# Performance work log

Measured on AMD Instinct MI355X. Metric: run time of the kernel, lower is better.

## Reference

```python
import jax, jax.numpy as jnp
import numpy as np

B, C, HID, H, W = 32, 256, 128, 32, 32  # batch, input_dim, hidden_dim, grid


def conv1x1(x, Wt, b):
    # 1x1 Conv2d == channel-mixing matmul. x: [B,Cin,H,W], Wt: [Cout,Cin]
    return jnp.einsum('oc,bchw->bohw', Wt, x) + b[None, :, None, None]


def setup_inputs() -> dict:
    key = jax.random.key(0)
    ks = jax.random.split(key, 18)
    p = lambda k, shape: (jax.random.normal(k, shape, jnp.float32) * 0.02)
    return {
        'h': jax.random.normal(ks[0], (B, C, H, W), jnp.float32),
        'm': jax.random.normal(ks[1], (B, C, H, W), jnp.float32),
        'Wq': p(ks[2], (HID, C)),  'bq': p(ks[3], (HID,)),
        'Wk': p(ks[4], (HID, C)),  'bk': p(ks[5], (HID,)),
        'Wv': p(ks[6], (C, C)),    'bv': p(ks[7], (C,)),
        'Wk2': p(ks[8], (HID, C)), 'bk2': p(ks[9], (HID,)),
        'Wv2': p(ks[10], (C, C)),  'bv2': p(ks[11], (C,)),
        'Wz': p(ks[12], (2 * C, 2 * C)), 'bz': p(ks[13], (2 * C,)),
        'Wm': p(ks[14], (3 * C, 3 * C)), 'bm': p(ks[15], (3 * C,)),
    }


def reference(h, m, Wq, bq, Wk, bk, Wv, bv, Wk2, bk2, Wv2, bv2, Wz, bz, Wm, bm):
    Bb, Cc, Hh, Ww = h.shape
    HW = Hh * Ww
    # shared query from h: [B, HID, HW]
    q = conv1x1(h, Wq, bq).reshape(Bb, -1, HW)
    # self-attention branch over h (unscaled logits, as in original)
    kh = conv1x1(h, Wk, bk).reshape(Bb, -1, HW)
    A_h = jax.nn.softmax(jnp.einsum('bdp,bdq->bpq', q, kh), axis=-1)  # [B,HW,HW]
    vh = conv1x1(h, Wv, bv).reshape(Bb, Cc, HW)
    Z_h = jnp.einsum('bpq,bcq->bcp', A_h, vh).reshape(Bb, Cc, Hh, Ww)
    # cross-attention branch over memory m with shared q
    km = conv1x1(m, Wk2, bk2).reshape(Bb, -1, HW)
    A_m = jax.nn.softmax(jnp.einsum('bdp,bdq->bpq', q, km), axis=-1)
    vm = conv1x1(m, Wv2, bv2).reshape(Bb, Cc, HW)
    Z_m = jnp.einsum('bpq,bcq->bcp', A_m, vm).reshape(Bb, Cc, Hh, Ww)
    # fuse, then LSTM-style gating
    Z = conv1x1(jnp.concatenate([Z_h, Z_m], axis=1), Wz, bz)          # [B,2C,H,W]
    comb = conv1x1(jnp.concatenate([Z, h], axis=1), Wm, bm)           # [B,3C,H,W]
    mo, mg, mi = jnp.split(comb, 3, axis=1)
    mi = jax.nn.sigmoid(mi)
    new_m = (1.0 - mi) * m + mi * jnp.tanh(mg)
    new_h = jax.nn.sigmoid(mo) * new_m
    return new_h, new_m
```

## Files before the change

kernel.cpp:

```cpp
#include <hip/hip_runtime.h>
#include <hip/hip_bf16.h>

typedef __bf16  v8bf __attribute__((ext_vector_type(8)));
typedef float   v4f  __attribute__((ext_vector_type(4)));
typedef float   f4   __attribute__((ext_vector_type(4)));
typedef unsigned short us8 __attribute__((ext_vector_type(8)));
typedef unsigned short us4 __attribute__((ext_vector_type(4)));
typedef unsigned int u32;

#define BATCH 32
#define CDIM  256
#define HW    1024

#define OFF_HBT 0L
#define OFF_MBT (OFF_HBT + 16777216L)
#define OFF_QKH (OFF_MBT + 16777216L)
#define OFF_QKM (OFF_QKH + 16777216L)
#define OFF_VH  (OFF_QKM + 8388608L)
#define OFF_VM  (OFF_VH  + 16777216L)
#define OFF_ZCT (OFF_VM  + 16777216L)
#define OFF_W   (OFF_ZCT + 33554432L)
#define OFF_B   (OFF_W   + 3866624L)
#define WS_TOTAL (OFF_B + 2944L * 4)
#define W_QK  0
#define W_K2  65536
#define W_V   98304
#define W_V2  163840
#define W_M   491520
#define W_ZT  1081344
#define W_F   1343488
#define B_QK  0
#define B_K2  256
#define B_V   384
#define B_V2  640
#define B_F   2176

__device__ inline unsigned short f2u(float x) {
    __hip_bfloat16 h = __float2bfloat16(x);
    union { __hip_bfloat16 h; unsigned short u; } cv; cv.h = h; return cv.u;
}
__device__ inline float u2f(unsigned short u) {
    union { unsigned short u; __hip_bfloat16 h; } cv; cv.u = u; return __bfloat162float(cv.h);
}
__device__ inline float sigmoidf_(float x) {
    x = fminf(fmaxf(x, -30.f), 30.f);
    return 1.f / (1.f + __expf(-x));
}
__device__ inline float tanhf_(float x) {
    x = fminf(fmaxf(x, -15.f), 15.f);
    float e = __expf(2.f * x);
    return (e - 1.f) / (e + 1.f);
}
__device__ inline void glds16(const unsigned short* g, unsigned short* l) {
    __builtin_amdgcn_global_load_lds(
        (const __attribute__((address_space(1))) u32*)g,
        (__attribute__((address_space(3))) u32*)l, 16, 0, 0);
}

__global__ __launch_bounds__(256)
void prep(const float* __restrict__ hsrc, const float* __restrict__ msrc,
          const float* __restrict__ Wq, const float* __restrict__ Wk,
          const float* __restrict__ Wv, const float* __restrict__ Wk2,
          const float* __restrict__ Wv2, const float* __restrict__ Wz,
          const float* __restrict__ Wm,
          const float* __restrict__ bq, const float* __restrict__ bk,
          const float* __restrict__ bk2, const float* __restrict__ bv,
          const float* __restrict__ bv2, const float* __restrict__ bz,
          const float* __restrict__ bm,
          char* __restrict__ ws)
{
    __shared__ float t[64][68];
    unsigned short* wdst = (unsigned short*)(ws + OFF_W);
    float*          bdst = (float*)(ws + OFF_B);
    const int bid = blockIdx.x;
    const int tid = threadIdx.x;

    if (bid < 6025) {
        const int gid = bid * 256 + tid;
        if (gid < 1081344) {
            const float* s; int off;
            if      (gid <   32768) { s = Wq;  off = gid; }
            else if (gid <   65536) { s = Wk;  off = gid -   32768; }
            else if (gid <   98304) { s = Wk2; off = gid -   65536; }
            else if (gid <  163840) { s = Wv;  off = gid -   98304; }
            else if (gid <  229376) { s = Wv2; off = gid -  163840; }
            else if (gid <  491520) { s = Wz;  off = gid -  229376; }
            else                    { s = Wm;  off = gid -  491520; }
            wdst[gid] = f2u(s[off]);
        } else if (gid < 1343488) {
            const int idx = gid - 1081344;
            const int k = idx >> 9, j = idx & 511;
            wdst[gid] = f2u(Wz[j * 512 + k]);
        } else if (gid < 1540096) {
            const int idx = gid - 1343488;
            const int o = idx >> 8, kk = 512 + (idx & 255);
            wdst[W_F + o * 768 + kk] = f2u(Wm[o * 768 + kk]);
        } else {
            const int bi = gid - 1540096;
            if (bi < 2176) {
                const float* s; int off;
                if      (bi <  128) { s = bq;  off = bi; }
                else if (bi <  256) { s = bk;  off = bi -  128; }
                else if (bi <  384) { s = bk2; off = bi -  256; }
                else if (bi <  640) { s = bv;  off = bi -  384; }
                else if (bi <  896) { s = bv2; off = bi -  640; }
                else if (bi < 1408) { s = bz;  off = bi -  896; }
                else                { s = bm;  off = bi - 1408; }
                bdst[bi] = s[off];
            }
        }
    } else if (bid < 6028) {
        const int o = (bid - 6025) * 256 + tid;
        if (o < 768) {
            float s = bm[o];
            const float* r = Wm + (long)o * 768;
#pragma unroll 8
            for (int j = 0; j < 512; ++j) s += r[j] * bz[j];
            bdst[B_F + o] = s;
        }
    } else {
        const int tz = bid - 6028;
        const int z  = tz >> 6;
        const int p0 = (tz & 15) * 64;
        const int c0 = ((tz >> 4) & 3) * 64;
        const float* src = (z < BATCH) ? hsrc + (long)z * CDIM * HW
                                       : msrc + (long)(z - BATCH) * CDIM * HW;
        unsigned short* dst = (unsigned short*)(ws + ((z < BATCH) ? OFF_HBT : OFF_MBT))
                              + (long)((z < BATCH) ? z : z - BATCH) * HW * CDIM;
        const int r  = tid >> 4;
        const int c4 = (tid & 15) * 4;
#pragma unroll
        for (int i = 0; i < 4; ++i) {
            const f4 v = *reinterpret_cast<const f4*>(src + (long)(c0 + r + 16 * i) * HW + p0 + c4);
            t[r + 16 * i][c4 + 0] = v[0];
            t[r + 16 * i][c4 + 1] = v[1];
            t[r + 16 * i][c4 + 2] = v[2];
            t[r + 16 * i][c4 + 3] = v[3];
        }
        __syncthreads();
#pragma unroll
        for (int i = 0; i < 4; ++i) {
            const int pr = r + 16 * i;
            us4 o;
#pragma unroll
            for (int j = 0; j < 4; ++j) o[j] = f2u(t[c4 + j][pr]);
            *reinterpret_cast<us4*>(dst + (long)(p0 + pr) * CDIM + c0 + c4) = o;
        }
    }
}

__device__ __forceinline__
void gemm_core(const unsigned short* __restrict__ A, int lda,
               const unsigned short* __restrict__ A2, int lda2, int kswitch,
               const unsigned short* __restrict__ Bt, int ldb,
               unsigned short* __restrict__ Cp, int ldc,
               int K, const float* __restrict__ bias, int biasMode,
               int m0, int n0,
               unsigned short* smem)
{
    unsigned short* As = smem;
    unsigned short* Bs = smem + 8192;

    const int tid  = threadIdx.x;
    const int lane = tid & 63;
    const int w    = tid >> 6;

    v4f acc[4][4];
#pragma unroll
    for (int i = 0; i < 4; ++i)
#pragma unroll
        for (int j = 0; j < 4; ++j) acc[i][j] = v4f{0.f, 0.f, 0.f, 0.f};

    const int wm   = (w >> 1) * 64;
    const int wn   = (w & 1) * 64;
    const int fr   = lane & 15;
    const int g    = lane >> 4;

    const int arow = (w << 3) + (lane >> 3);
    const int acol = (((lane & 7) ^ ((lane >> 3) & 7)) * 8);
    const int lbase = (w << 9);

    for (int k0 = 0; k0 < K; k0 += 64) {
        const unsigned short* Ab; int Al; int Ao;
        if (k0 < kswitch) { Ab = A;  Al = lda;  Ao = k0; }
        else              { Ab = A2; Al = lda2; Ao = k0 - kswitch; }
        const unsigned short* ga = Ab + (long)(m0 + arow) * Al + Ao + acol;
        const unsigned short* gb = Bt + (long)(n0 + arow) * ldb + k0 + acol;
#pragma unroll
        for (int i = 0; i < 4; ++i) {
            glds16(ga + (long)(32 * i) * Al, &As[i * 2048 + lbase]);
            glds16(gb + (long)(32 * i) * ldb, &Bs[i * 2048 + lbase]);
        }
        __syncthreads();
#pragma unroll
        for (int ks = 0; ks < 2; ++ks) {
            const int slot = ((ks * 4 + g) ^ (fr & 7)) * 8;
            v8bf af[4], bfv[4];
#pragma unroll
            for (int mi = 0; mi < 4; ++mi)
                af[mi] = *reinterpret_cast<const v8bf*>(&As[(wm + mi * 16 + fr) * 64 + slot]);
#pragma unroll
            for (int ni = 0; ni < 4; ++ni)
                bfv[ni] = *reinterpret_cast<const v8bf*>(&Bs[(wn + ni * 16 + fr) * 64 + slot]);
#pragma unroll
            for (int mi = 0; mi < 4; ++mi)
#pragma unroll
                for (int ni = 0; ni < 4; ++ni)
                    acc[mi][ni] = __builtin_amdgcn_mfma_f32_16x16x32_bf16(af[mi], bfv[ni], acc[mi][ni], 0, 0, 0);
        }
        __syncthreads();
    }

    unsigned short* Cs = smem;
#pragma unroll
    for (int mi = 0; mi < 4; ++mi) {
#pragma unroll
        for (int ni = 0; ni < 4; ++ni) {
            const int col = wn + ni * 16 + fr;
            const int rb  = wm + mi * 16 + g * 4;
            const float bn = (biasMode == 1) ? bias[n0 + col] : 0.f;
#pragma unroll
            for (int r = 0; r < 4; ++r) {
                float x = acc[mi][ni][r] + bn;
                if (biasMode == 2) x += bias[m0 + rb + r];
                Cs[(rb + r) * 132 + col] = f2u(x);
            }
        }
    }
    __syncthreads();

    const int orow = tid >> 4;
    const int och  = (tid & 15) * 8;
#pragma unroll
    for (int i = 0; i < 8; ++i) {
        const int row = i * 16 + orow;
        *reinterpret_cast<us8*>(Cp + (long)(m0 + row) * ldc + n0 + och) =
            *reinterpret_cast<const us8*>(&Cs[row * 132 + och]);
    }
    __syncthreads();
}

__global__ __launch_bounds__(256)
void gemm_multi(char* __restrict__ ws)
{
    __shared__ unsigned short smem[16896];
    unsigned short* wA = (unsigned short*)(ws + OFF_W);
    float*          bA = (float*)(ws + OFF_B);
    const int id = blockIdx.x;

    if (id < 512) {
        const int b = id >> 4, x = id & 7, y = (id >> 3) & 1;
        const unsigned short* A = (unsigned short*)(ws + OFF_HBT) + (long)b * 262144;
        gemm_core(A, 256, A, 256, 1 << 30, wA + W_QK, 256,
                  (unsigned short*)(ws + OFF_QKH) + (long)b * 262144, 256,
                  256, bA + B_QK, 1, x * 128, y * 128, smem);
    } else if (id < 768) {
        const int idx = id - 512, b = idx >> 3, x = idx & 7;
        const unsigned short* A = (unsigned short*)(ws + OFF_MBT) + (long)b * 262144;
        gemm_core(A, 256, A, 256, 1 << 30, wA + W_K2, 256,
                  (unsigned short*)(ws + OFF_QKM) + (long)b * 131072, 128,
                  256, bA + B_K2, 1, x * 128, 0, smem);
    } else if (id < 1280) {
        const int idx = id - 768, b = idx >> 4, x = idx & 1, y = (idx >> 1) & 7;
        gemm_core(wA + W_V, 256, wA + W_V, 256, 1 << 30,
                  (unsigned short*)(ws + OFF_HBT) + (long)b * 262144, 256,
                  (unsigned short*)(ws + OFF_VH) + (long)b * 262144, 1024,
                  256, bA + B_V, 2, x * 128, y * 128, smem);
    } else if (id < 1792) {
        const int idx = id - 1280, b = idx >> 4, x = idx & 1, y = (idx >> 1) & 7;
        gemm_core(wA + W_V2, 256, wA + W_V2, 256, 1 << 30,
                  (unsigned short*)(ws + OFF_MBT) + (long)b * 262144, 256,
                  (unsigned short*)(ws + OFF_VM) + (long)b * 262144, 1024,
                  256, bA + B_V2, 2, x * 128, y * 128, smem);
    } else {
        const int idx = id - 1792, x = idx % 6, y = idx / 6;
        gemm_core(wA + W_M, 768, wA + W_M, 768, 1 << 30, wA + W_ZT, 512,
                  wA + W_F, 768, 512, bA, 0, x * 128, y * 128, smem);
    }
}

__global__ __launch_bounds__(512, 2)
void comb_gemm(const unsigned short* __restrict__ A, int lda,
               const unsigned short* __restrict__ A2, int lda2, int kswitch,
               const unsigned short* __restrict__ Bt, int ldb,
               int K, const float* __restrict__ bias,
               const float* __restrict__ mIn,
               float* __restrict__ outh, float* __restrict__ outm)
{
    __shared__ unsigned short smem[57344];

    const int nwg = gridDim.x;
    const int wg  = (blockIdx.x & 7) * (nwg >> 3) + (blockIdx.x >> 3);
    const int m0  = (wg >> 2) * 256;
    const int c0  = (wg & 3) * 64;

    const int tid  = threadIdx.x;
    const int lane = tid & 63;
    const int w    = tid >> 6;
    const int fr   = lane & 15;
    const int g    = lane >> 4;
    const int wm   = (w >> 2) * 128;
    const int wn   = (w & 3) * 48;

    const int srow   = tid >> 3;
    const int schunk = ((tid & 7) ^ (srow & 7)) * 8;
    const int sdst   = w * 512;

    v4f acc[8][3];
#pragma unroll
    for (int i = 0; i < 8; ++i)
#pragma unroll
        for (int j = 0; j < 3; ++j) acc[i][j] = v4f{0.f, 0.f, 0.f, 0.f};

    const int nt = K >> 6;

#define STAGE_A(t, bi, i)                                                      \
    { const int k0 = (t) * 64;                                                 \
      const unsigned short* Ab; int Al; int Ao;                                \
      if (k0 < kswitch) { Ab = A;  Al = lda;  Ao = k0; }                       \
      else              { Ab = A2; Al = lda2; Ao = k0 - kswitch; }             \
      glds16(Ab + (long)(m0 + (i) * 64 + srow) * Al + Ao + schunk,             \
             &smem[(bi) * 16384 + (i) * 4096 + sdst]); }
#define STAGE_B(t, bi, i)                                                      \
    { const int k0 = (t) * 64;                                                 \
      glds16(Bt + (long)((i) * 256 + c0 + srow) * ldb + k0 + schunk,           \
             &smem[32768 + (bi) * 12288 + (i) * 4096 + sdst]); }

#pragma unroll
    for (int i = 0; i < 4; ++i) STAGE_A(0, 0, i);
#pragma unroll
    for (int i = 0; i < 3; ++i) STAGE_B(0, 0, i);

    for (int t = 0; t < nt; ++t) {
        __syncthreads();

        const unsigned short* Ar = smem + (t & 1) * 16384;
        const unsigned short* Br = smem + 32768 + (t & 1) * 12288;
        const int nb = (t + 1) & 1;
        const bool more = (t + 1 < nt);

#pragma unroll
        for (int ks = 0; ks < 2; ++ks) {
            v8bf bf[3];
#pragma unroll
            for (int ni = 0; ni < 3; ++ni) {
                const int r = wn + ni * 16 + fr;
                bf[ni] = *reinterpret_cast<const v8bf*>(
                    &Br[r * 64 + ((ks * 4 + g) ^ (r & 7)) * 8]);
            }
#pragma unroll
            for (int hh = 0; hh < 2; ++hh) {
                v8bf af[4];
#pragma unroll
                for (int mi = 0; mi < 4; ++mi) {
                    const int r = wm + (hh * 4 + mi) * 16 + fr;
                    af[mi] = *reinterpret_cast<const v8bf*>(
                        &Ar[r * 64 + ((ks * 4 + g) ^ (r & 7)) * 8]);
                }
                if (more) {
                    const int ph = ks * 2 + hh;
                    if (ph == 0)      { STAGE_A(t + 1, nb, 0); STAGE_A(t + 1, nb, 1); }
                    else if (ph == 1) { STAGE_A(t + 1, nb, 2); STAGE_A(t + 1, nb, 3); }
                    else if (ph == 2) { STAGE_B(t + 1, nb, 0); STAGE_B(t + 1, nb, 1); }
                    else              { STAGE_B(t + 1, nb, 2); }
                }
                __builtin_amdgcn_s_setprio(1);
#pragma unroll
                for (int mi = 0; mi < 4; ++mi)
#pragma unroll
                    for (int ni = 0; ni < 3; ++ni)
                        acc[hh * 4 + mi][ni] = __builtin_amdgcn_mfma_f32_16x16x32_bf16(
                            af[mi], bf[ni], acc[hh * 4 + mi][ni], 0, 0, 0);
                __builtin_amdgcn_s_setprio(0);
            }
        }
    }
#undef STAGE_A
#undef STAGE_B

    __syncthreads();

    unsigned short* Lt = smem;
#pragma unroll
    for (int mi = 0; mi < 8; ++mi) {
#pragma unroll
        for (int ni = 0; ni < 3; ++ni) {
            const int j  = wn + ni * 16 + fr;
            const int cg = ((j >> 6) << 8) + c0 + (j & 63);
            const float bn = bias[cg];
            const int rl = wm + mi * 16 + g * 4;
#pragma unroll
            for (int r = 0; r < 4; ++r)
                Lt[(rl + r) * 194 + j] = f2u(acc[mi][ni][r] + bn);
        }
    }
    __syncthreads();

    const int b     = m0 >> 10;
    const int pbase = m0 & 1023;
    const int pl    = tid & 255;
    const int ch    = tid >> 8;
#pragma unroll 4
    for (int cc = 0; cc < 32; ++cc) {
        const int cl = ch * 32 + cc;
        const float mo  = u2f(Lt[pl * 194 + cl]);
        const float mg  = u2f(Lt[pl * 194 + 64 + cl]);
        const float mi_ = u2f(Lt[pl * 194 + 128 + cl]);
        const long gi = ((long)(b * 256 + c0 + cl)) * 1024 + pbase + pl;
        const float mv = mIn[gi];
        const float ms = sigmoidf_(mi_);
        const float nm = (1.f - ms) * mv + ms * tanhf_(mg);
        const float nh = sigmoidf_(mo) * nm;
        outh[gi] = nh;
        outm[gi] = nm;
    }
}

__global__ __launch_bounds__(512, 4)
void attn_fused(const unsigned short* __restrict__ Qb, long sQ, int ldq,
                const unsigned short* __restrict__ K0, long sK0, int ldk0,
                const unsigned short* __restrict__ V0,
                const unsigned short* __restrict__ K1, long sK1, int ldk1,
                const unsigned short* __restrict__ V1,
                unsigned short* __restrict__ Out, long sO)
{
    __shared__ unsigned short Qs[128 * 128];
    __shared__ unsigned short Ks[32 * 128];
    __shared__ unsigned short Vs[256 * 32];
    __shared__ unsigned short Ps[128 * 32];

    const int id = blockIdx.x;
    const int c8 = id & 7;
    const int k  = id >> 3;
    const int z  = c8 * 8 + (k >> 3);
    const int p0 = (k & 7) * 128;

    const int b  = (z < 32) ? z : z - 32;
    const unsigned short* Kp; const unsigned short* Vp; int ldk, outoff;
    if (z < 32) { Kp = K0 + (long)b * sK0; Vp = V0 + (long)b * 262144L; ldk = ldk0; outoff = 0; }
    else        { Kp = K1 + (long)b * sK1; Vp = V1 + (long)b * 262144L; ldk = ldk1; outoff = 256; }
    const unsigned short* Qp = Qb + (long)b * sQ;
    Out += (long)b * sO;

    const int tid  = threadIdx.x;
    const int lane = tid & 63;
    const int w    = tid >> 6;
    const int fr   = lane & 15;
    const int g    = lane >> 4;
    const int wp   = w >> 2;
    const int wq   = w & 3;
    const int srow0 = wp * 64 + (wq >> 1) * 32;
    const int kc0   = (wq & 1) * 16;
    const int kr    = kc0 + fr;
    const int wc    = wq * 64;

    v4f vacc[4][4];
#pragma unroll
    for (int i = 0; i < 4; ++i)
#pragma unroll
        for (int j = 0; j < 4; ++j) vacc[i][j] = v4f{0.f, 0.f, 0.f, 0.f};
    float rp[2][4];
#pragma unroll
    for (int i = 0; i < 2; ++i)
#pragma unroll
        for (int r = 0; r < 4; ++r) rp[i][r] = 0.f;

    const int qkrow  = tid >> 4;
    const int qkchk  = ((tid & 15) ^ (qkrow & 7)) * 8;
    const int vrow   = tid >> 2;
    const int vchk   = ((tid & 3) ^ ((vrow >> 1) & 3)) * 8;
    const int sdst   = w * 512;

#define STAGE_Q()                                                              \
    { _Pragma("unroll")                                                        \
      for (int i = 0; i < 4; ++i)                                              \
          glds16(Qp + (long)(p0 + i * 32 + qkrow) * ldq + qkchk,               \
                 &Qs[i * 4096 + sdst]); }
#define STAGE_K(t)                                                             \
    glds16(Kp + (long)((t) * 32 + qkrow) * ldk + qkchk, &Ks[sdst]);
#define STAGE_V(t)                                                             \
    { const int kv0 = (t) * 32;                                                \
      _Pragma("unroll")                                                        \
      for (int i = 0; i < 2; ++i)                                              \
          glds16(Vp + (long)(i * 128 + vrow) * 1024 + kv0 + vchk,              \
                 &Vs[i * 4096 + sdst]); }

    STAGE_Q();
    STAGE_K(0);

    for (int t = 0; t < 32; ++t) {
        __syncthreads();
        STAGE_V(t);

        v4f sacc[2];
#pragma unroll
        for (int mi = 0; mi < 2; ++mi) sacc[mi] = v4f{0.f, 0.f, 0.f, 0.f};
        __builtin_amdgcn_s_setprio(1);
#pragma unroll
        for (int ks = 0; ks < 4; ++ks) {
            const v8bf kf = *reinterpret_cast<const v8bf*>(
                &Ks[kr * 128 + ((ks * 4 + g) ^ (kr & 7)) * 8]);
#pragma unroll
            for (int mi = 0; mi < 2; ++mi) {
                const int qrow = srow0 + mi * 16 + fr;
                const v8bf qf = *reinterpret_cast<const v8bf*>(
                    &Qs[qrow * 128 + ((ks * 4 + g) ^ (qrow & 7)) * 8]);
                sacc[mi] = __builtin_amdgcn_mfma_f32_16x16x32_bf16(qf, kf, sacc[mi], 0, 0, 0);
            }
        }
        __builtin_amdgcn_s_setprio(0);
#pragma unroll
        for (int mi = 0; mi < 2; ++mi)
#pragma unroll
            for (int r = 0; r < 4; ++r) {
                const float e = __expf(sacc[mi][r]);
                rp[mi][r] += e;
                const int prow = srow0 + mi * 16 + g * 4 + r;
                Ps[prow * 32 + (((kr >> 3) ^ ((prow >> 1) & 3)) << 3) + (kr & 7)] = f2u(e);
            }

        __syncthreads();
        if (t < 31) STAGE_K(t + 1);

        __builtin_amdgcn_s_setprio(1);
        {
            v8bf pf[4], vf[4];
#pragma unroll
            for (int mi = 0; mi < 4; ++mi) {
                const int pr = wp * 64 + mi * 16 + fr;
                pf[mi] = *reinterpret_cast<const v8bf*>(
                    &Ps[pr * 32 + ((g ^ ((pr >> 1) & 3)) << 3)]);
            }
#pragma unroll
            for (int ni = 0; ni < 4; ++ni) {
                const int vr = wc + ni * 16 + fr;
                vf[ni] = *reinterpret_cast<const v8bf*>(
                    &Vs[vr * 32 + ((g ^ ((vr >> 1) & 3)) << 3)]);
            }
#pragma unroll
            for (int mi = 0; mi < 4; ++mi)
#pragma unroll
                for (int ni = 0; ni < 4; ++ni)
                    vacc[mi][ni] = __builtin_amdgcn_mfma_f32_16x16x32_bf16(pf[mi], vf[ni], vacc[mi][ni], 0, 0, 0);
        }
        __builtin_amdgcn_s_setprio(0);
    }
#undef STAGE_Q
#undef STAGE_K
#undef STAGE_V

    __syncthreads();
    float* red = reinterpret_cast<float*>(Ps);
#pragma unroll
    for (int mi = 0; mi < 2; ++mi)
#pragma unroll
        for (int r = 0; r < 4; ++r) {
            float v = rp[mi][r];
            v += __shfl_xor(v, 1);
            v += __shfl_xor(v, 2);
            v += __shfl_xor(v, 4);
            v += __shfl_xor(v, 8);
            if (fr == 0) red[(wq & 1) * 128 + srow0 + mi * 16 + g * 4 + r] = v;
        }
    __syncthreads();

#pragma unroll
    for (int mi = 0; mi < 4; ++mi)
#pragma unroll
        for (int r = 0; r < 4; ++r) {
            const int pl = wp * 64 + mi * 16 + g * 4 + r;
            const float inv = 1.f / (red[pl] + red[128 + pl]);
#pragma unroll
            for (int ni = 0; ni < 4; ++ni)
                Out[(long)(p0 + pl) * 512 + outoff + wc + ni * 16 + fr]
                    = f2u(vacc[mi][ni][r] * inv);
        }
}

extern "C" void kernel_launch(void* const* d_in, const int* in_sizes, int n_in,
                              void* d_out, int out_size, void* d_ws, size_t ws_size,
                              hipStream_t stream)
{
    const float* h   = (const float*)d_in[0];
    const float* m   = (const float*)d_in[1];
    const float* Wq  = (const float*)d_in[2];
    const float* bq  = (const float*)d_in[3];
    const float* Wk  = (const float*)d_in[4];
    const float* bk  = (const float*)d_in[5];
    const float* Wv  = (const float*)d_in[6];
    const float* bv  = (const float*)d_in[7];
    const float* Wk2 = (const float*)d_in[8];
    const float* bk2 = (const float*)d_in[9];
    const float* Wv2 = (const float*)d_in[10];
    const float* bv2 = (const float*)d_in[11];
    const float* Wz  = (const float*)d_in[12];
    const float* bz  = (const float*)d_in[13];
    const float* Wm  = (const float*)d_in[14];
    const float* bm  = (const float*)d_in[15];

    char* ws = (char*)d_ws;
    if (ws_size < (size_t)WS_TOTAL) return;

    unsigned short* hT  = (unsigned short*)(ws + OFF_HBT);
    unsigned short* qkh = (unsigned short*)(ws + OFF_QKH);
    unsigned short* qkm = (unsigned short*)(ws + OFF_QKM);
    unsigned short* vh  = (unsigned short*)(ws + OFF_VH);
    unsigned short* vm  = (unsigned short*)(ws + OFF_VM);
    unsigned short* zct = (unsigned short*)(ws + OFF_ZCT);
    unsigned short* wA  = (unsigned short*)(ws + OFF_W);
    float*          bA  = (float*)(ws + OFF_B);

    float* outh = (float*)d_out;
    float* outm = outh + 8388608L;

    prep<<<dim3(10124), dim3(256), 0, stream>>>(
        h, m, Wq, Wk, Wv, Wk2, Wv2, Wz, Wm,
        bq, bk, bk2, bv, bv2, bz, bm, ws);

    gemm_multi<<<dim3(1816), dim3(256), 0, stream>>>(ws);

    attn_fused<<<dim3(512), dim3(512), 0, stream>>>(
        qkh, 262144L, 256,
        qkh + 128, 262144L, 256, vh,
        qkm, 131072L, 128, vm,
        zct, 524288L);

    comb_gemm<<<dim3(512), dim3(512), 0, stream>>>(
        zct, 512, hT, 256, 512,
        wA + W_F, 768, 768, bA + B_F, m, outh, outm);
}
```

Baseline: 200.0 us.

## Double-buffer LDS tiles in GEMM core and prefetch next K-tile during MFMA

Turns the GEMM main loop into a two-stage LDS pipeline. The next K-tile's A and B global-to-LDS loads are issued while the current tile's MFMAs run, and the loop needs one barrier per iteration instead of two. Wave priority is also raised around the MFMA block. Shared memory per block doubles to 64KB, which may limit occupancy, and correctness depends on the async LDS loads completing before the next barrier.

```diff
diff --git a/kernel.cpp b/kernel.cpp
--- a/kernel.cpp
+++ b/kernel.cpp
@@ -158,9 +158,6 @@
                int m0, int n0,
                unsigned short* smem)
 {
-    unsigned short* As = smem;
-    unsigned short* Bs = smem + 8192;
-
     const int tid  = threadIdx.x;
     const int lane = tid & 63;
     const int w    = tid >> 6;
@@ -180,36 +177,60 @@
     const int acol = (((lane & 7) ^ ((lane >> 3) & 7)) * 8);
     const int lbase = (w << 9);
 
-    for (int k0 = 0; k0 < K; k0 += 64) {
-        const unsigned short* Ab; int Al; int Ao;
-        if (k0 < kswitch) { Ab = A;  Al = lda;  Ao = k0; }
-        else              { Ab = A2; Al = lda2; Ao = k0 - kswitch; }
-        const unsigned short* ga = Ab + (long)(m0 + arow) * Al + Ao + acol;
-        const unsigned short* gb = Bt + (long)(n0 + arow) * ldb + k0 + acol;
-#pragma unroll
-        for (int i = 0; i < 4; ++i) {
-            glds16(ga + (long)(32 * i) * Al, &As[i * 2048 + lbase]);
-            glds16(gb + (long)(32 * i) * ldb, &Bs[i * 2048 + lbase]);
-        }
+    const int nt = K >> 6;
+
+#define GSTAGE_A(t, bi, i)                                                     \
+    { const int k0 = (t) * 64;                                                 \
+      const unsigned short* Ab; int Al; int Ao;                                \
+      if (k0 < kswitch) { Ab = A;  Al = lda;  Ao = k0; }                       \
+      else              { Ab = A2; Al = lda2; Ao = k0 - kswitch; }             \
+      glds16(Ab + (long)(m0 + (i) * 32 + arow) * Al + Ao + acol,               \
+             &smem[(bi) * 8192 + (i) * 2048 + lbase]); }
+#define GSTAGE_B(t, bi, i)                                                     \
+    { const int k0 = (t) * 64;                                                 \
+      glds16(Bt + (long)(n0 + (i) * 32 + arow) * ldb + k0 + acol,              \
+             &smem[16384 + (bi) * 8192 + (i) * 2048 + lbase]); }
+
+#pragma unroll
+    for (int i = 0; i < 4; ++i) { GSTAGE_A(0, 0, i); GSTAGE_B(0, 0, i); }
+
+    for (int t = 0; t < nt; ++t) {
         __syncthreads();
+
+        const unsigned short* Ar = smem + (t & 1) * 8192;
+        const unsigned short* Br = smem + 16384 + (t & 1) * 8192;
+        const int nb = (t + 1) & 1;
+        const bool more = (t + 1 < nt);
+
 #pragma unroll
         for (int ks = 0; ks < 2; ++ks) {
             const int slot = ((ks * 4 + g) ^ (fr & 7)) * 8;
             v8bf af[4], bfv[4];
 #pragma unroll
             for (int mi = 0; mi < 4; ++mi)
-                af[mi] = *reinterpret_cast<const v8bf*>(&As[(wm + mi * 16 + fr) * 64 + slot]);
+                af[mi] = *reinterpret_cast<const v8bf*>(&Ar[(wm + mi * 16 + fr) * 64 + slot]);
 #pragma unroll
             for (int ni = 0; ni < 4; ++ni)
-                bfv[ni] = *reinterpret_cast<const v8bf*>(&Bs[(wn + ni * 16 + fr) * 64 + slot]);
+                bfv[ni] = *reinterpret_cast<const v8bf*>(&Br[(wn + ni * 16 + fr) * 64 + slot]);
+            if (more) {
+                if (ks == 0) { GSTAGE_A(t + 1, nb, 0); GSTAGE_A(t + 1, nb, 1);
+                               GSTAGE_A(t + 1, nb, 2); GSTAGE_A(t + 1, nb, 3); }
+                else         { GSTAGE_B(t + 1, nb, 0); GSTAGE_B(t + 1, nb, 1);
+                               GSTAGE_B(t + 1, nb, 2); GSTAGE_B(t + 1, nb, 3); }
+            }
+            __builtin_amdgcn_s_setprio(1);
 #pragma unroll
             for (int mi = 0; mi < 4; ++mi)
 #pragma unroll
                 for (int ni = 0; ni < 4; ++ni)
                     acc[mi][ni] = __builtin_amdgcn_mfma_f32_16x16x32_bf16(af[mi], bfv[ni], acc[mi][ni], 0, 0, 0);
-        }
-        __syncthreads();
-    }
+            __builtin_amdgcn_s_setprio(0);
+        }
+    }
+#undef GSTAGE_A
+#undef GSTAGE_B
+
+    __syncthreads();
 
     unsigned short* Cs = smem;
 #pragma unroll
@@ -237,13 +258,12 @@
         *reinterpret_cast<us8*>(Cp + (long)(m0 + row) * ldc + n0 + och) =
             *reinterpret_cast<const us8*>(&Cs[row * 132 + och]);
     }
-    __syncthreads();
 }
 
 __global__ __launch_bounds__(256)
 void gemm_multi(char* __restrict__ ws)
 {
-    __shared__ unsigned short smem[16896];
+    __shared__ unsigned short smem[32768];
     unsigned short* wA = (unsigned short*)(ws + OFF_W);
     float*          bA = (float*)(ws + OFF_B);
     const int id = blockIdx.x;
```

Measured after the change: 203.8 us. Within noise of the previous version (+1.9%).
